# Kernel optimization log

Measured on AMD Instinct MI355X. Metric: run time of the kernel, lower is better.

Reference implementation:

```python
import jax, jax.numpy as jnp
import numpy as np

N, E, D, R, L = 50000, 600000, 64, 65, 2


def setup_inputs() -> dict:
    key = jax.random.key(0)
    ks = jax.random.split(key, 10)
    x = jax.random.normal(ks[0], (N, D), dtype=jnp.float32)
    edge_index = jax.random.randint(ks[1], (2, E), 0, N, dtype=jnp.int64)
    edge_type = jax.random.randint(ks[2], (E,), 0, R, dtype=jnp.int64)
    s = 1.0 / np.sqrt(D)
    W = jax.random.normal(ks[3], (L, R, D, D), dtype=jnp.float32) * s
    root = jax.random.normal(ks[4], (L, D, D), dtype=jnp.float32) * s
    bias = jax.random.normal(ks[5], (L, D), dtype=jnp.float32) * 0.01
    res_W = jax.random.normal(ks[6], (L, D, D), dtype=jnp.float32) * s
    res_b = jax.random.normal(ks[7], (L, D), dtype=jnp.float32) * 0.01
    return {"x": x, "edge_index": edge_index, "edge_type": edge_type,
            "W": W, "root": root, "bias": bias, "res_W": res_W, "res_b": res_b}


def _rgcn_conv(x, src, dst, edge_type, W_r, W_root, b):
    # PyG RGCNConv (num_bases=None, aggr='mean'):
    #   out_i = x_i @ W_root + b + sum_r mean_{j in N_r(i)} (x_j @ W_r)
    # mean is linear, so aggregate raw features per (node, relation) first,
    # then apply the per-relation transform once per node.
    n, d = x.shape
    r = W_r.shape[0]
    seg = dst * r + edge_type                       # [E]
    msg = x[src]                                    # [E, D] gather
    agg = jax.ops.segment_sum(msg, seg, num_segments=n * r).reshape(n, r, d)
    cnt = jax.ops.segment_sum(jnp.ones((msg.shape[0],), x.dtype), seg,
                              num_segments=n * r).reshape(n, r, 1)
    mean = agg / jnp.maximum(cnt, 1.0)              # [N, R, D]
    out = jnp.einsum('nrd,rdk->nk', mean, W_r)
    return out + x @ W_root + b


def reference(x, edge_index, edge_type, W, root, bias, res_W, res_b):
    src, dst = edge_index[0], edge_index[1]
    h = x
    for l in range(W.shape[0]):
        conv = _rgcn_conv(h, src, dst, edge_type, W[l], root[l], bias[l])
        conv = jax.nn.relu(conv)
        # dropout: identity in eval mode
        res = jax.nn.relu(h @ res_W[l] + res_b[l])
        h = conv + res
    return h
```

## Files before the change

### kernel.cpp

```cpp
#include <hip/hip_runtime.h>


constexpr int NN  = 50000;
constexpr int EE  = 600000;
constexpr int DIM = 64;
constexpr int RR  = 65;
constexpr int CHUNK = 256;
constexpr int MAXCHUNKS = EE / CHUNK + RR + 8;
constexpr int SORT_BS = 2048;
constexpr int NSB = (EE + SORT_BS - 1) / SORT_BS;
constexpr int SCAN_BS = 1024;
constexpr int SCAN_NB = (NN + SCAN_BS - 1) / SCAN_BS;
constexpr int XNB = 64;

typedef __attribute__((ext_vector_type(8))) short short8v;
typedef __attribute__((ext_vector_type(4))) float floatx4;

__device__ inline unsigned short f2bf(float f) {
  unsigned int u = __float_as_uint(f);
  return (unsigned short)((u + 0x7fffu + ((u >> 16) & 1u)) >> 16);
}
__device__ inline float bf2f(unsigned short v) {
  return __uint_as_float(((unsigned int)v) << 16);
}


__global__ __launch_bounds__(512) void cnt_k(const int* __restrict__ dst,
                                             const int* __restrict__ et,
                                             int* __restrict__ cnt, int E) {
  const int e = blockIdx.x * 512 + threadIdx.x;
  if (e < E) atomicAdd(&cnt[et[e] * NN + dst[e]], 1);
}

__global__ __launch_bounds__(512) void bhist_k(const int* __restrict__ et,
                                               int* __restrict__ bhist, int E) {
  __shared__ int lh[RR];
  for (int i = threadIdx.x; i < RR; i += 512) lh[i] = 0;
  __syncthreads();
  const int base = blockIdx.x * SORT_BS;
  for (int i = threadIdx.x; i < SORT_BS; i += 512) {
    const int e = base + i;
    if (e < E) atomicAdd(&lh[et[e]], 1);
  }
  __syncthreads();
  for (int i = threadIdx.x; i < RR; i += 512) bhist[blockIdx.x * RR + i] = lh[i];
}


__global__ __launch_bounds__(1024) void scan1_k(const int* __restrict__ cnt,
                                                int* __restrict__ deg,
                                                int* __restrict__ bsum) {
  __shared__ int s[SCAN_BS];
  const int idx = blockIdx.x * SCAN_BS + threadIdx.x;
  int d = 0;
  if (idx < NN) {
#pragma unroll 13
    for (int r = 0; r < RR; ++r) d += cnt[r * NN + idx];
    deg[idx] = d;
  }
  s[threadIdx.x] = d;
  __syncthreads();
  for (int off = SCAN_BS / 2; off > 0; off >>= 1) {
    if (threadIdx.x < off) s[threadIdx.x] += s[threadIdx.x + off];
    __syncthreads();
  }
  if (threadIdx.x == 0) bsum[blockIdx.x] = s[0];
}

__global__ __launch_bounds__(64) void scan2_k(int* __restrict__ bsum) {
  if (threadIdx.x == 0) {
    int run = 0;
    for (int b = 0; b < SCAN_NB; ++b) { const int v = bsum[b]; bsum[b] = run; run += v; }
  }
}

__global__ __launch_bounds__(1024) void scan3_k(const int* __restrict__ deg,
                                                const int* __restrict__ bsum,
                                                int* __restrict__ rowptr,
                                                int* __restrict__ poscur) {
  __shared__ int s[SCAN_BS];
  const int t = threadIdx.x;
  const int idx = blockIdx.x * SCAN_BS + t;
  const int v = (idx < NN) ? deg[idx] : 0;
  s[t] = v;
  __syncthreads();
  for (int off = 1; off < SCAN_BS; off <<= 1) {
    const int u = (t >= off) ? s[t - off] : 0;
    __syncthreads();
    s[t] += u;
    __syncthreads();
  }
  const int excl = bsum[blockIdx.x] + s[t] - v;
  if (idx < NN) { rowptr[idx] = excl; poscur[idx] = excl; }
  if (idx == NN - 1) rowptr[NN] = EE;
}

__global__ __launch_bounds__(128) void scan_type_k(const int* __restrict__ bhist,
                                                   int* __restrict__ boff,
                                                   int4* __restrict__ chunkArr,
                                                   int* __restrict__ nchunks) {
  __shared__ int total[RR], tptr[RR + 1], chbase[RR + 1];
  const int t = threadIdx.x;
  if (t < RR) {
    int s = 0;
    for (int b = 0; b < NSB; ++b) s += bhist[b * RR + t];
    total[t] = s;
  }
  __syncthreads();
  if (t == 0) {
    int run = 0, crun = 0;
    for (int r = 0; r < RR; ++r) {
      tptr[r] = run;   run  += total[r];
      chbase[r] = crun; crun += (total[r] + CHUNK - 1) / CHUNK;
    }
    tptr[RR] = run; chbase[RR] = crun;
    *nchunks = crun;
  }
  __syncthreads();
  if (t < RR) {
    int run = tptr[t];
    for (int b = 0; b < NSB; ++b) { boff[b * RR + t] = run; run += bhist[b * RR + t]; }
    const int nc = (total[t] + CHUNK - 1) / CHUNK;
    for (int i = 0; i < nc; ++i) {
      const int beg = tptr[t] + i * CHUNK;
      chunkArr[chbase[t] + i] = make_int4(beg, min(beg + CHUNK, tptr[t] + total[t]), t, 0);
    }
  }
}

__global__ __launch_bounds__(512) void scatter_k(const int* __restrict__ src,
                                                 const int* __restrict__ dst,
                                                 const int* __restrict__ et,
                                                 const int* __restrict__ cnt,
                                                 const int* __restrict__ boff,
                                                 int* __restrict__ poscur,
                                                 int* __restrict__ osrc,
                                                 int* __restrict__ opos,
                                                 float* __restrict__ oscale, int E) {
  __shared__ int cur[RR];
  for (int i = threadIdx.x; i < RR; i += 512) cur[i] = boff[blockIdx.x * RR + i];
  __syncthreads();
  const int base = blockIdx.x * SORT_BS;
  for (int i = threadIdx.x; i < SORT_BS; i += 512) {
    const int e = base + i;
    if (e < E) {
      const int s = src[e], d = dst[e], r = et[e];
      const int q = atomicAdd(&cur[r], 1);
      const int p = atomicAdd(&poscur[d], 1);
      osrc[q] = s;
      opos[q] = p;
      oscale[q] = 1.0f / (float)cnt[r * NN + d];
    }
  }
}


__global__ __launch_bounds__(256) void cvtw_k(const float* __restrict__ W,
                                              unsigned short* __restrict__ WT) {
  const int tid = blockIdx.x * 256 + threadIdx.x;
  const int total4 = 2 * RR * DIM * DIM / 4;
  if (tid >= total4) return;
  const int base = tid * 4;
  const int mat = base >> 12;
  const int rem = base & 4095;
  const int k = rem >> 6, c0 = rem & 63;
  const float4 v = *reinterpret_cast<const float4*>(W + base);
  unsigned short* o = WT + (size_t)mat * 4096;
  o[(c0 + 0) * 64 + k] = f2bf(v.x);
  o[(c0 + 1) * 64 + k] = f2bf(v.y);
  o[(c0 + 2) * 64 + k] = f2bf(v.z);
  o[(c0 + 3) * 64 + k] = f2bf(v.w);
}


__global__ __launch_bounds__(256) void msgm_k(const unsigned short* __restrict__ hbf,
                                              const int* __restrict__ osrc,
                                              const int* __restrict__ opos,
                                              const float* __restrict__ oscale,
                                              const unsigned short* __restrict__ WT,
                                              const int4* __restrict__ chunkArr,
                                              const int* __restrict__ nchunks,
                                              unsigned short* __restrict__ m) {
  const int ci = blockIdx.x;
  if (ci >= *nchunks) return;
  const int4 c = chunkArr[ci];
  const int beg = c.x, end = c.y, rel = c.z;

  __shared__ unsigned short Wl[DIM][72];
  {
    const float4* s4 = reinterpret_cast<const float4*>(WT + (size_t)rel * 4096);
#pragma unroll
    for (int it = 0; it < 2; ++it) {
      const int seg = threadIdx.x + it * 256;
      const int row = seg >> 3, s8 = seg & 7;
      *reinterpret_cast<float4*>(&Wl[row][s8 * 8]) = s4[seg];
    }
  }
  __syncthreads();

  const int w  = threadIdx.x >> 6;
  const int l  = threadIdx.x & 63;
  const int lr = l & 15, lq = l >> 4;

  const int ebase = beg + w * 64;
  if (ebase >= end) return;

  short8v a[4][2];
#pragma unroll
  for (int ct = 0; ct < 4; ++ct)
#pragma unroll
    for (int kk = 0; kk < 2; ++kk)
      a[ct][kk] = *reinterpret_cast<const short8v*>(&Wl[ct * 16 + lr][kk * 32 + lq * 8]);

  short8v b[4][2];
  int eidx[4];
#pragma unroll
  for (int et = 0; et < 4; ++et) {
    eidx[et] = ebase + et * 16 + lr;
    const int e = min(eidx[et], end - 1);
    const int s = osrc[e];
    const unsigned short* hp = hbf + (size_t)s * DIM;
    b[et][0] = *reinterpret_cast<const short8v*>(hp + lq * 8);
    b[et][1] = *reinterpret_cast<const short8v*>(hp + 32 + lq * 8);
  }

  floatx4 acc[4][4];
#pragma unroll
  for (int ct = 0; ct < 4; ++ct)
#pragma unroll
    for (int et = 0; et < 4; ++et)
      acc[ct][et] = (floatx4){0.f, 0.f, 0.f, 0.f};

#pragma unroll
  for (int kk = 0; kk < 2; ++kk)
#pragma unroll
    for (int ct = 0; ct < 4; ++ct)
#pragma unroll
      for (int et = 0; et < 4; ++et)
        acc[ct][et] = __builtin_amdgcn_mfma_f32_16x16x32_bf16(a[ct][kk], b[et][kk],
                                                              acc[ct][et], 0, 0, 0);

#pragma unroll
  for (int et = 0; et < 4; ++et) {
    const int e = eidx[et];
    if (e < end) {
      const float sc = oscale[e];
      unsigned short* op = m + (size_t)opos[e] * DIM;
#pragma unroll
      for (int ct = 0; ct < 4; ++ct) {
        ushort4 o;
        o.x = f2bf(acc[ct][et][0] * sc);
        o.y = f2bf(acc[ct][et][1] * sc);
        o.z = f2bf(acc[ct][et][2] * sc);
        o.w = f2bf(acc[ct][et][3] * sc);
        *reinterpret_cast<ushort4*>(op + ct * 16 + lq * 4) = o;
      }
    }
  }
}

__global__ __launch_bounds__(256) void msg_k(const float* __restrict__ h,
                                             const int* __restrict__ osrc,
                                             const int* __restrict__ opos,
                                             const float* __restrict__ oscale,
                                             const float* __restrict__ W,
                                             const int4* __restrict__ chunkArr,
                                             const int* __restrict__ nchunks,
                                             unsigned short* __restrict__ m) {
  const int ci = blockIdx.x;
  if (ci >= *nchunks) return;
  const int4 c = chunkArr[ci];
  const int beg = c.x, end = c.y, rel = c.z;

  __shared__ float Wlds[DIM * DIM];
  const float* Wg = W + (size_t)rel * (DIM * DIM);
#pragma unroll
  for (int i = 0; i < 4; ++i)
    *reinterpret_cast<float4*>(&Wlds[i * 1024 + threadIdx.x * 4]) =
        *reinterpret_cast<const float4*>(Wg + i * 1024 + threadIdx.x * 4);
  __syncthreads();

  const int g = threadIdx.x >> 4, li = threadIdx.x & 15;
  __shared__ float xs[16][4][68];

  for (int b = 0; b < 4; ++b) {
    const int e0 = beg + g * 16 + b * 4;
    const int nvalid = min(4, end - e0);
    if (nvalid <= 0) continue;

#pragma unroll
    for (int r = 0; r < 4; ++r) {
      const int e = e0 + ((r < nvalid) ? r : (nvalid - 1));
      const int s = osrc[e];
      *reinterpret_cast<float4*>(&xs[g][r][li * 4]) =
          *reinterpret_cast<const float4*>(h + (size_t)s * DIM + li * 4);
    }

    float acc[4][4];
#pragma unroll
    for (int r = 0; r < 4; ++r) { acc[r][0] = 0.f; acc[r][1] = 0.f; acc[r][2] = 0.f; acc[r][3] = 0.f; }

#pragma unroll 8
    for (int k = 0; k < DIM; ++k) {
      const float4 w = *reinterpret_cast<const float4*>(&Wlds[k * DIM + li * 4]);
#pragma unroll
      for (int r = 0; r < 4; ++r) {
        const float xv = xs[g][r][k];
        acc[r][0] += xv * w.x; acc[r][1] += xv * w.y;
        acc[r][2] += xv * w.z; acc[r][3] += xv * w.w;
      }
    }

    for (int r = 0; r < nvalid; ++r) {
      const int e = e0 + r;
      const float sc = oscale[e];
      ushort4 o;
      o.x = f2bf(acc[r][0] * sc); o.y = f2bf(acc[r][1] * sc);
      o.z = f2bf(acc[r][2] * sc); o.w = f2bf(acc[r][3] * sc);
      *reinterpret_cast<ushort4*>(m + (size_t)opos[e] * DIM + li * 4) = o;
    }
  }
}

__global__ __launch_bounds__(256) void xform_k(const float* __restrict__ h,
                                               const float* __restrict__ root,
                                               const float* __restrict__ bias,
                                               const float* __restrict__ rw,
                                               const float* __restrict__ rb,
                                               float* __restrict__ rt,
                                               float* __restrict__ rs,
                                               unsigned short* __restrict__ hbf, int N) {
  __shared__ float Wl0[DIM * DIM];
  __shared__ float Wl1[DIM * DIM];
  __shared__ float xs[XNB][68];
#pragma unroll
  for (int i = 0; i < 4; ++i) {
    reinterpret_cast<float4*>(Wl0)[threadIdx.x + i * 256] =
        reinterpret_cast<const float4*>(root)[threadIdx.x + i * 256];
    reinterpret_cast<float4*>(Wl1)[threadIdx.x + i * 256] =
        reinterpret_cast<const float4*>(rw)[threadIdx.x + i * 256];
  }

  const int g = threadIdx.x >> 4, li = threadIdx.x & 15;
  const int base = blockIdx.x * XNB;
#pragma unroll
  for (int r = 0; r < 4; ++r) {
    const int n = base + g * 4 + r;
    float4 v = make_float4(0.f, 0.f, 0.f, 0.f);
    if (n < N) v = *reinterpret_cast<const float4*>(h + (size_t)n * DIM + li * 4);
    *reinterpret_cast<float4*>(&xs[g * 4 + r][li * 4]) = v;
  }
  __syncthreads();

  if (hbf != nullptr) {
#pragma unroll
    for (int r = 0; r < 4; ++r) {
      const int n = base + g * 4 + r;
      if (n < N) {
        const float4 v = *reinterpret_cast<const float4*>(&xs[g * 4 + r][li * 4]);
        ushort4 o;
        o.x = f2bf(v.x); o.y = f2bf(v.y); o.z = f2bf(v.z); o.w = f2bf(v.w);
        *reinterpret_cast<ushort4*>(hbf + (size_t)n * DIM + li * 4) = o;
      }
    }
  }

  float aR[4][4], aS[4][4];
#pragma unroll
  for (int r = 0; r < 4; ++r)
#pragma unroll
    for (int q = 0; q < 4; ++q) { aR[r][q] = 0.f; aS[r][q] = 0.f; }

#pragma unroll 4
  for (int k = 0; k < DIM; ++k) {
    const float4 wr = *reinterpret_cast<const float4*>(&Wl0[k * DIM + li * 4]);
    const float4 wv = *reinterpret_cast<const float4*>(&Wl1[k * DIM + li * 4]);
#pragma unroll
    for (int r = 0; r < 4; ++r) {
      const float xv = xs[g * 4 + r][k];
      aR[r][0] += xv * wr.x; aR[r][1] += xv * wr.y; aR[r][2] += xv * wr.z; aR[r][3] += xv * wr.w;
      aS[r][0] += xv * wv.x; aS[r][1] += xv * wv.y; aS[r][2] += xv * wv.z; aS[r][3] += xv * wv.w;
    }
  }

  const float4 bv = reinterpret_cast<const float4*>(bias)[li];
  const float4 cv = reinterpret_cast<const float4*>(rb)[li];
#pragma unroll
  for (int r = 0; r < 4; ++r) {
    const int n = base + g * 4 + r;
    if (n < N) {
      *reinterpret_cast<float4*>(rt + (size_t)n * DIM + li * 4) =
          make_float4(aR[r][0] + bv.x, aR[r][1] + bv.y, aR[r][2] + bv.z, aR[r][3] + bv.w);
      *reinterpret_cast<float4*>(rs + (size_t)n * DIM + li * 4) =
          make_float4(fmaxf(aS[r][0] + cv.x, 0.f), fmaxf(aS[r][1] + cv.y, 0.f),
                      fmaxf(aS[r][2] + cv.z, 0.f), fmaxf(aS[r][3] + cv.w, 0.f));
    }
  }
}

__global__ __launch_bounds__(256) void gather2_k(const unsigned short* __restrict__ m,
                                                 const int* __restrict__ rowptr,
                                                 const float* __restrict__ rt,
                                                 const float* __restrict__ rs,
                                                 float* __restrict__ hout, int N) {
  const int g = threadIdx.x >> 4, li = threadIdx.x & 15;
  const int n = blockIdx.x * 16 + g;
  if (n >= N) return;

  float a0 = 0.f, a1 = 0.f, a2 = 0.f, a3 = 0.f;
  const int jb = rowptr[n], je = rowptr[n + 1];
  int j = jb;
  for (; j + 4 <= je; j += 4) {
    const ushort4 v0 = *reinterpret_cast<const ushort4*>(m + (size_t)(j + 0) * DIM + li * 4);
    const ushort4 v1 = *reinterpret_cast<const ushort4*>(m + (size_t)(j + 1) * DIM + li * 4);
    const ushort4 v2 = *reinterpret_cast<const ushort4*>(m + (size_t)(j + 2) * DIM + li * 4);
    const ushort4 v3 = *reinterpret_cast<const ushort4*>(m + (size_t)(j + 3) * DIM + li * 4);
    a0 += bf2f(v0.x) + bf2f(v1.x) + bf2f(v2.x) + bf2f(v3.x);
    a1 += bf2f(v0.y) + bf2f(v1.y) + bf2f(v2.y) + bf2f(v3.y);
    a2 += bf2f(v0.z) + bf2f(v1.z) + bf2f(v2.z) + bf2f(v3.z);
    a3 += bf2f(v0.w) + bf2f(v1.w) + bf2f(v2.w) + bf2f(v3.w);
  }
  for (; j < je; ++j) {
    const ushort4 v = *reinterpret_cast<const ushort4*>(m + (size_t)j * DIM + li * 4);
    a0 += bf2f(v.x); a1 += bf2f(v.y); a2 += bf2f(v.z); a3 += bf2f(v.w);
  }

  const float4 t = *reinterpret_cast<const float4*>(rt + (size_t)n * DIM + li * 4);
  const float4 s = *reinterpret_cast<const float4*>(rs + (size_t)n * DIM + li * 4);
  *reinterpret_cast<float4*>(hout + (size_t)n * DIM + li * 4) =
      make_float4(fmaxf(a0 + t.x, 0.f) + s.x, fmaxf(a1 + t.y, 0.f) + s.y,
                  fmaxf(a2 + t.z, 0.f) + s.z, fmaxf(a3 + t.w, 0.f) + s.w);
}

__global__ __launch_bounds__(256) void gather_k(const float* __restrict__ hin,
                                                const unsigned short* __restrict__ m,
                                                const int* __restrict__ rowptr,
                                                const float* __restrict__ root,
                                                const float* __restrict__ bias,
                                                const float* __restrict__ rw,
                                                const float* __restrict__ rb,
                                                float* __restrict__ hout, int N) {
  __shared__ float xs[16][68];
  const int g = threadIdx.x >> 4, li = threadIdx.x & 15;
  const int n = blockIdx.x * 16 + g;
  if (n >= N) return;

  *reinterpret_cast<float4*>(&xs[g][li * 4]) =
      *reinterpret_cast<const float4*>(hin + (size_t)n * DIM + li * 4);

  float a0 = 0.f, a1 = 0.f, a2 = 0.f, a3 = 0.f;
  const int jb = rowptr[n], je = rowptr[n + 1];
  for (int j = jb; j < je; ++j) {
    const ushort4 mv = *reinterpret_cast<const ushort4*>(m + (size_t)j * DIM + li * 4);
    a0 += bf2f(mv.x); a1 += bf2f(mv.y); a2 += bf2f(mv.z); a3 += bf2f(mv.w);
  }

  float r0 = 0.f, r1 = 0.f, r2 = 0.f, r3 = 0.f;
  float s0 = 0.f, s1 = 0.f, s2 = 0.f, s3 = 0.f;
#pragma unroll 8
  for (int k = 0; k < DIM; ++k) {
    const float hd = xs[g][k];
    const float4 w = *reinterpret_cast<const float4*>(root + k * DIM + li * 4);
    const float4 v = *reinterpret_cast<const float4*>(rw + k * DIM + li * 4);
    r0 += hd * w.x; r1 += hd * w.y; r2 += hd * w.z; r3 += hd * w.w;
    s0 += hd * v.x; s1 += hd * v.y; s2 += hd * v.z; s3 += hd * v.w;
  }
  const float4 b = *reinterpret_cast<const float4*>(bias + li * 4);
  const float4 cc = *reinterpret_cast<const float4*>(rb + li * 4);
  float o0 = fmaxf(a0 + r0 + b.x, 0.f) + fmaxf(s0 + cc.x, 0.f);
  float o1 = fmaxf(a1 + r1 + b.y, 0.f) + fmaxf(s1 + cc.y, 0.f);
  float o2 = fmaxf(a2 + r2 + b.z, 0.f) + fmaxf(s2 + cc.z, 0.f);
  float o3 = fmaxf(a3 + r3 + b.w, 0.f) + fmaxf(s3 + cc.w, 0.f);
  *reinterpret_cast<float4*>(hout + (size_t)n * DIM + li * 4) = make_float4(o0, o1, o2, o3);
}


__global__ __launch_bounds__(256) void count_k(const int* __restrict__ dst,
                                               const int* __restrict__ et,
                                               int* __restrict__ cnt, int E) {
  int e = blockIdx.x * 256 + threadIdx.x;
  if (e < E) atomicAdd(&cnt[dst[e] * RR + et[e]], 1);
}

__global__ __launch_bounds__(256) void edge_k(const float* __restrict__ h,
                                              const int* __restrict__ src,
                                              const int* __restrict__ dst,
                                              const int* __restrict__ et,
                                              const float* __restrict__ W,
                                              const int* __restrict__ cnt,
                                              float* __restrict__ accum, int E) {
  __shared__ float xs[16][68];
  const int g = threadIdx.x >> 4, li = threadIdx.x & 15;
  const int e = blockIdx.x * 16 + g;
  if (e >= E) return;
  const int s = src[e], d = dst[e], t = et[e];
  *reinterpret_cast<float4*>(&xs[g][li * 4]) =
      *reinterpret_cast<const float4*>(h + (size_t)s * DIM + li * 4);
  const float* Wt = W + (size_t)t * (DIM * DIM) + li * 4;
  float a0 = 0.f, a1 = 0.f, a2 = 0.f, a3 = 0.f;
#pragma unroll 8
  for (int k = 0; k < DIM; ++k) {
    const float xd = xs[g][k];
    const float4 w = *reinterpret_cast<const float4*>(Wt + k * DIM);
    a0 += xd * w.x; a1 += xd * w.y; a2 += xd * w.z; a3 += xd * w.w;
  }
  const float sc = 1.0f / (float)cnt[d * RR + t];
  float* o = accum + (size_t)d * DIM + li * 4;
  unsafeAtomicAdd(o + 0, a0 * sc);
  unsafeAtomicAdd(o + 1, a1 * sc);
  unsafeAtomicAdd(o + 2, a2 * sc);
  unsafeAtomicAdd(o + 3, a3 * sc);
}

__global__ __launch_bounds__(256) void node_k(const float* __restrict__ h,
                                              const float* __restrict__ root,
                                              const float* __restrict__ bias,
                                              const float* __restrict__ rw,
                                              const float* __restrict__ rb,
                                              float* __restrict__ io, int N) {
  __shared__ float xs[16][68];
  const int g = threadIdx.x >> 4, li = threadIdx.x & 15;
  const int n = blockIdx.x * 16 + g;
  if (n >= N) return;
  *reinterpret_cast<float4*>(&xs[g][li * 4]) =
      *reinterpret_cast<const float4*>(h + (size_t)n * DIM + li * 4);
  float r0 = 0.f, r1 = 0.f, r2 = 0.f, r3 = 0.f;
  float s0 = 0.f, s1 = 0.f, s2 = 0.f, s3 = 0.f;
#pragma unroll 8
  for (int k = 0; k < DIM; ++k) {
    const float hd = xs[g][k];
    const float4 w = *reinterpret_cast<const float4*>(root + k * DIM + li * 4);
    const float4 v = *reinterpret_cast<const float4*>(rw + k * DIM + li * 4);
    r0 += hd * w.x; r1 += hd * w.y; r2 += hd * w.z; r3 += hd * w.w;
    s0 += hd * v.x; s1 += hd * v.y; s2 += hd * v.z; s3 += hd * v.w;
  }
  float* o = io + (size_t)n * DIM + li * 4;
  const float4 acc = *reinterpret_cast<const float4*>(o);
  const float4 b = *reinterpret_cast<const float4*>(bias + li * 4);
  const float4 c = *reinterpret_cast<const float4*>(rb + li * 4);
  float o0 = fmaxf(acc.x + r0 + b.x, 0.f) + fmaxf(s0 + c.x, 0.f);
  float o1 = fmaxf(acc.y + r1 + b.y, 0.f) + fmaxf(s1 + c.y, 0.f);
  float o2 = fmaxf(acc.z + r2 + b.z, 0.f) + fmaxf(s2 + c.z, 0.f);
  float o3 = fmaxf(acc.w + r3 + b.w, 0.f) + fmaxf(s3 + c.w, 0.f);
  *reinterpret_cast<float4*>(o) = make_float4(o0, o1, o2, o3);
}


extern "C" void kernel_launch(void* const* d_in, const int* in_sizes, int n_in,
                              void* d_out, int out_size, void* d_ws, size_t ws_size,
                              hipStream_t stream) {
  const float* x    = (const float*)d_in[0];
  const int*   ei   = (const int*)d_in[1];
  const int*   et   = (const int*)d_in[2];
  const float* W    = (const float*)d_in[3];
  const float* root = (const float*)d_in[4];
  const float* bias = (const float*)d_in[5];
  const float* resW = (const float*)d_in[6];
  const float* resb = (const float*)d_in[7];
  float* out = (float*)d_out;

  const int* src = ei;
  const int* dstp = ei + EE;

  char* ws = (char*)d_ws;
  size_t off = 0;
  auto take = [&](size_t bytes) -> void* {
    void* p = ws + off;
    off = (off + bytes + 255) & ~(size_t)255;
    return p;
  };
  unsigned short* m = (unsigned short*)take((size_t)EE * DIM * sizeof(unsigned short));
  float* h1      = (float*)take((size_t)NN * DIM * sizeof(float));
  int* deg       = (int*)take((size_t)NN * sizeof(int));
  int* rowptr    = (int*)take((size_t)(NN + 1) * sizeof(int));
  int* poscur    = (int*)take((size_t)NN * sizeof(int));
  int* bhist     = (int*)take((size_t)NSB * RR * sizeof(int));
  int* boff      = (int*)take((size_t)NSB * RR * sizeof(int));
  int* bsum      = (int*)take((size_t)SCAN_NB * sizeof(int));
  int* osrc      = (int*)take((size_t)EE * sizeof(int));
  int* opos      = (int*)take((size_t)EE * sizeof(int));
  float* oscale  = (float*)take((size_t)EE * sizeof(float));
  int4* chunkArr = (int4*)take((size_t)MAXCHUNKS * sizeof(int4));
  int* nchunks   = (int*)take(256);
  const size_t base_off = off;
  float* rt      = (float*)take((size_t)NN * DIM * sizeof(float));
  float* rs      = (float*)take((size_t)NN * DIM * sizeof(float));
  const size_t t1_off = off;
  unsigned short* hbf = (unsigned short*)take((size_t)NN * DIM * sizeof(unsigned short));
  unsigned short* wbt = (unsigned short*)take((size_t)2 * RR * DIM * DIM * sizeof(unsigned short));
  const size_t mfma_off = off;
  int* cnt       = (int*)m;

  if (base_off <= ws_size) {
    hipMemsetAsync(cnt, 0, (size_t)NN * RR * sizeof(int), stream);

    cnt_k<<<(EE + 511) / 512, 512, 0, stream>>>(dstp, et, cnt, EE);
    bhist_k<<<NSB, 512, 0, stream>>>(et, bhist, EE);
    scan1_k<<<SCAN_NB, 1024, 0, stream>>>(cnt, deg, bsum);
    scan2_k<<<1, 64, 0, stream>>>(bsum);
    scan3_k<<<SCAN_NB, 1024, 0, stream>>>(deg, bsum, rowptr, poscur);
    scan_type_k<<<1, 128, 0, stream>>>(bhist, boff, chunkArr, nchunks);
    scatter_k<<<NSB, 512, 0, stream>>>(src, dstp, et, cnt, boff, poscur,
                                       osrc, opos, oscale, EE);

    const int XG = (NN + XNB - 1) / XNB;
    if (mfma_off <= ws_size) {
      cvtw_k<<<(2 * RR * DIM * DIM / 4 + 255) / 256, 256, 0, stream>>>(W, wbt);
      xform_k<<<XG, 256, 0, stream>>>(x, root, bias, resW, resb, rt, rs, hbf, NN);
      msgm_k<<<MAXCHUNKS, 256, 0, stream>>>(hbf, osrc, opos, oscale, wbt, chunkArr, nchunks, m);
      gather2_k<<<(NN + 15) / 16, 256, 0, stream>>>(m, rowptr, rt, rs, h1, NN);
      xform_k<<<XG, 256, 0, stream>>>(h1, root + DIM * DIM, bias + DIM,
                                      resW + DIM * DIM, resb + DIM, rt, rs, hbf, NN);
      msgm_k<<<MAXCHUNKS, 256, 0, stream>>>(hbf, osrc, opos, oscale,
                                            wbt + (size_t)RR * DIM * DIM, chunkArr, nchunks, m);
      gather2_k<<<(NN + 15) / 16, 256, 0, stream>>>(m, rowptr, rt, rs, out, NN);
    } else if (t1_off <= ws_size) {
      msg_k<<<MAXCHUNKS, 256, 0, stream>>>(x, osrc, opos, oscale, W, chunkArr, nchunks, m);
      xform_k<<<XG, 256, 0, stream>>>(x, root, bias, resW, resb, rt, rs, nullptr, NN);
      gather2_k<<<(NN + 15) / 16, 256, 0, stream>>>(m, rowptr, rt, rs, h1, NN);
      msg_k<<<MAXCHUNKS, 256, 0, stream>>>(h1, osrc, opos, oscale,
                                           W + (size_t)RR * DIM * DIM, chunkArr, nchunks, m);
      xform_k<<<XG, 256, 0, stream>>>(h1, root + DIM * DIM, bias + DIM,
                                      resW + DIM * DIM, resb + DIM, rt, rs, nullptr, NN);
      gather2_k<<<(NN + 15) / 16, 256, 0, stream>>>(m, rowptr, rt, rs, out, NN);
    } else {
      msg_k<<<MAXCHUNKS, 256, 0, stream>>>(x, osrc, opos, oscale, W, chunkArr, nchunks, m);
      gather_k<<<(NN + 15) / 16, 256, 0, stream>>>(x, m, rowptr, root, bias, resW, resb, h1, NN);
      msg_k<<<MAXCHUNKS, 256, 0, stream>>>(h1, osrc, opos, oscale,
                                           W + (size_t)RR * DIM * DIM, chunkArr, nchunks, m);
      gather_k<<<(NN + 15) / 16, 256, 0, stream>>>(h1, m, rowptr, root + DIM * DIM, bias + DIM,
                                                   resW + DIM * DIM, resb + DIM, out, NN);
    }
  } else {
    int* fcnt = (int*)ws;
    float* fh1 = (float*)(ws + (size_t)NN * RR * sizeof(int));
    hipMemsetAsync(fcnt, 0, (size_t)NN * RR * sizeof(int), stream);
    hipMemsetAsync(fh1, 0, (size_t)NN * DIM * sizeof(float), stream);
    hipMemsetAsync(out, 0, (size_t)NN * DIM * sizeof(float), stream);
    count_k<<<(EE + 255) / 256, 256, 0, stream>>>(dstp, et, fcnt, EE);
    edge_k<<<(EE + 15) / 16, 256, 0, stream>>>(x, src, dstp, et, W, fcnt, fh1, EE);
    node_k<<<(NN + 15) / 16, 256, 0, stream>>>(x, root, bias, resW, resb, fh1, NN);
    edge_k<<<(EE + 15) / 16, 256, 0, stream>>>(fh1, src, dstp, et,
                                               W + (size_t)RR * DIM * DIM, fcnt, out, EE);
    node_k<<<(NN + 15) / 16, 256, 0, stream>>>(fh1, root + DIM * DIM, bias + DIM,
                                               resW + DIM * DIM, resb + DIM, out, NN);
  }
}
```

Before: 273.0 us.

## Replace dense per-(node,relation) count array with per-node degree and local relation counts

Drops the NN×RR count array, which needed a 13MB memset, scattered atomics and a 65-way strided reduction for degrees. Degrees now come from a per-node atomic histogram fused with the relation block histogram. Mean scales are recomputed per destination segment by a quadratic scan over relation ids and applied in the gather instead of the message kernel. It also halves the sort block size and removes the non-MFMA fallback paths, which adds an extra kernel and an extra per-edge array.

```diff
diff --git a/kernel.cpp b/kernel.cpp
--- a/kernel.cpp
+++ b/kernel.cpp
@@ -7,7 +7,7 @@
 constexpr int RR  = 65;
 constexpr int CHUNK = 256;
 constexpr int MAXCHUNKS = EE / CHUNK + RR + 8;
-constexpr int SORT_BS = 2048;
+constexpr int SORT_BS = 1024;
 constexpr int NSB = (EE + SORT_BS - 1) / SORT_BS;
 constexpr int SCAN_BS = 1024;
 constexpr int SCAN_NB = (NN + SCAN_BS - 1) / SCAN_BS;
@@ -25,40 +25,37 @@
 }
 
 
-__global__ __launch_bounds__(512) void cnt_k(const int* __restrict__ dst,
-                                             const int* __restrict__ et,
-                                             int* __restrict__ cnt, int E) {
-  const int e = blockIdx.x * 512 + threadIdx.x;
-  if (e < E) atomicAdd(&cnt[et[e] * NN + dst[e]], 1);
-}
-
-__global__ __launch_bounds__(512) void bhist_k(const int* __restrict__ et,
+__global__ __launch_bounds__(256) void zero_k(int* __restrict__ p, int n) {
+  const int i = blockIdx.x * 256 + threadIdx.x;
+  if (i < n) p[i] = 0;
+}
+
+__global__ __launch_bounds__(512) void hist2_k(const int* __restrict__ dst,
+                                               const int* __restrict__ et,
+                                               int* __restrict__ deg,
                                                int* __restrict__ bhist, int E) {
   __shared__ int lh[RR];
-  for (int i = threadIdx.x; i < RR; i += 512) lh[i] = 0;
+  if (threadIdx.x < RR) lh[threadIdx.x] = 0;
   __syncthreads();
   const int base = blockIdx.x * SORT_BS;
-  for (int i = threadIdx.x; i < SORT_BS; i += 512) {
-    const int e = base + i;
-    if (e < E) atomicAdd(&lh[et[e]], 1);
-  }
-  __syncthreads();
-  for (int i = threadIdx.x; i < RR; i += 512) bhist[blockIdx.x * RR + i] = lh[i];
-}
-
-
-__global__ __launch_bounds__(1024) void scan1_k(const int* __restrict__ cnt,
-                                                int* __restrict__ deg,
+#pragma unroll
+  for (int it = 0; it < SORT_BS / 512; ++it) {
+    const int e = base + it * 512 + threadIdx.x;
+    if (e < E) {
+      atomicAdd(&deg[dst[e]], 1);
+      atomicAdd(&lh[et[e]], 1);
+    }
+  }
+  __syncthreads();
+  if (threadIdx.x < RR) bhist[blockIdx.x * RR + threadIdx.x] = lh[threadIdx.x];
+}
+
+
+__global__ __launch_bounds__(1024) void scan1_k(const int* __restrict__ deg,
                                                 int* __restrict__ bsum) {
   __shared__ int s[SCAN_BS];
   const int idx = blockIdx.x * SCAN_BS + threadIdx.x;
-  int d = 0;
-  if (idx < NN) {
-#pragma unroll 13
-    for (int r = 0; r < RR; ++r) d += cnt[r * NN + idx];
-    deg[idx] = d;
-  }
-  s[threadIdx.x] = d;
+  s[threadIdx.x] = (idx < NN) ? deg[idx] : 0;
   __syncthreads();
   for (int off = SCAN_BS / 2; off > 0; off >>= 1) {
     if (threadIdx.x < off) s[threadIdx.x] += s[threadIdx.x + off];
@@ -128,29 +125,43 @@
   }
 }
 
-__global__ __launch_bounds__(512) void scatter_k(const int* __restrict__ src,
-                                                 const int* __restrict__ dst,
-                                                 const int* __restrict__ et,
-                                                 const int* __restrict__ cnt,
-                                                 const int* __restrict__ boff,
-                                                 int* __restrict__ poscur,
-                                                 int* __restrict__ osrc,
-                                                 int* __restrict__ opos,
-                                                 float* __restrict__ oscale, int E) {
+__global__ __launch_bounds__(512) void scatter2_k(const int* __restrict__ src,
+                                                  const int* __restrict__ dst,
+                                                  const int* __restrict__ et,
+                                                  const int* __restrict__ boff,
+                                                  int* __restrict__ poscur,
+                                                  int* __restrict__ osrc,
+                                                  int* __restrict__ opos,
+                                                  int* __restrict__ orel, int E) {
   __shared__ int cur[RR];
-  for (int i = threadIdx.x; i < RR; i += 512) cur[i] = boff[blockIdx.x * RR + i];
+  if (threadIdx.x < RR) cur[threadIdx.x] = boff[blockIdx.x * RR + threadIdx.x];
   __syncthreads();
   const int base = blockIdx.x * SORT_BS;
-  for (int i = threadIdx.x; i < SORT_BS; i += 512) {
-    const int e = base + i;
+#pragma unroll
+  for (int it = 0; it < SORT_BS / 512; ++it) {
+    const int e = base + it * 512 + threadIdx.x;
     if (e < E) {
       const int s = src[e], d = dst[e], r = et[e];
       const int q = atomicAdd(&cur[r], 1);
       const int p = atomicAdd(&poscur[d], 1);
       osrc[q] = s;
       opos[q] = p;
-      oscale[q] = 1.0f / (float)cnt[r * NN + d];
-    }
+      orel[p] = r;
+    }
+  }
+}
+
+__global__ __launch_bounds__(256) void scale_k(const int* __restrict__ rowptr,
+                                               const int* __restrict__ orel,
+                                               float* __restrict__ sc, int N) {
+  const int n = blockIdx.x * 256 + threadIdx.x;
+  if (n >= N) return;
+  const int jb = rowptr[n], je = rowptr[n + 1];
+  for (int j1 = jb; j1 < je; ++j1) {
+    const int r1 = orel[j1];
+    int c = 0;
+    for (int j2 = jb; j2 < je; ++j2) c += (orel[j2] == r1) ? 1 : 0;
+    sc[j1] = 1.0f / (float)c;
   }
 }
 
@@ -176,7 +187,6 @@
 __global__ __launch_bounds__(256) void msgm_k(const unsigned short* __restrict__ hbf,
                                               const int* __restrict__ osrc,
                                               const int* __restrict__ opos,
-                                              const float* __restrict__ oscale,
                                               const unsigned short* __restrict__ WT,
                                               const int4* __restrict__ chunkArr,
                                               const int* __restrict__ nchunks,
@@ -244,80 +254,16 @@
   for (int et = 0; et < 4; ++et) {
     const int e = eidx[et];
     if (e < end) {
-      const float sc = oscale[e];
       unsigned short* op = m + (size_t)opos[e] * DIM;
 #pragma unroll
       for (int ct = 0; ct < 4; ++ct) {
         ushort4 o;
-        o.x = f2bf(acc[ct][et][0] * sc);
-        o.y = f2bf(acc[ct][et][1] * sc);
-        o.z = f2bf(acc[ct][et][2] * sc);
-        o.w = f2bf(acc[ct][et][3] * sc);
+        o.x = f2bf(acc[ct][et][0]);
+        o.y = f2bf(acc[ct][et][1]);
+        o.z = f2bf(acc[ct][et][2]);
+        o.w = f2bf(acc[ct][et][3]);
         *reinterpret_cast<ushort4*>(op + ct * 16 + lq * 4) = o;
       }
-    }
-  }
-}
-
-__global__ __launch_bounds__(256) void msg_k(const float* __restrict__ h,
-                                             const int* __restrict__ osrc,
-                                             const int* __restrict__ opos,
-                                             const float* __restrict__ oscale,
-                                             const float* __restrict__ W,
-                                             const int4* __restrict__ chunkArr,
-                                             const int* __restrict__ nchunks,
-                                             unsigned short* __restrict__ m) {
-  const int ci = blockIdx.x;
-  if (ci >= *nchunks) return;
-  const int4 c = chunkArr[ci];
-  const int beg = c.x, end = c.y, rel = c.z;
-
-  __shared__ float Wlds[DIM * DIM];
-  const float* Wg = W + (size_t)rel * (DIM * DIM);
-#pragma unroll
-  for (int i = 0; i < 4; ++i)
-    *reinterpret_cast<float4*>(&Wlds[i * 1024 + threadIdx.x * 4]) =
-        *reinterpret_cast<const float4*>(Wg + i * 1024 + threadIdx.x * 4);
-  __syncthreads();
-
-  const int g = threadIdx.x >> 4, li = threadIdx.x & 15;
-  __shared__ float xs[16][4][68];
-
-  for (int b = 0; b < 4; ++b) {
-    const int e0 = beg + g * 16 + b * 4;
-    const int nvalid = min(4, end - e0);
-    if (nvalid <= 0) continue;
-
-#pragma unroll
-    for (int r = 0; r < 4; ++r) {
-      const int e = e0 + ((r < nvalid) ? r : (nvalid - 1));
-      const int s = osrc[e];
-      *reinterpret_cast<float4*>(&xs[g][r][li * 4]) =
-          *reinterpret_cast<const float4*>(h + (size_t)s * DIM + li * 4);
-    }
-
-    float acc[4][4];
-#pragma unroll
-    for (int r = 0; r < 4; ++r) { acc[r][0] = 0.f; acc[r][1] = 0.f; acc[r][2] = 0.f; acc[r][3] = 0.f; }
-
-#pragma unroll 8
-    for (int k = 0; k < DIM; ++k) {
-      const float4 w = *reinterpret_cast<const float4*>(&Wlds[k * DIM + li * 4]);
-#pragma unroll
-      for (int r = 0; r < 4; ++r) {
-        const float xv = xs[g][r][k];
-        acc[r][0] += xv * w.x; acc[r][1] += xv * w.y;
-        acc[r][2] += xv * w.z; acc[r][3] += xv * w.w;
-      }
-    }
-
-    for (int r = 0; r < nvalid; ++r) {
-      const int e = e0 + r;
-      const float sc = oscale[e];
-      ushort4 o;
-      o.x = f2bf(acc[r][0] * sc); o.y = f2bf(acc[r][1] * sc);
-      o.z = f2bf(acc[r][2] * sc); o.w = f2bf(acc[r][3] * sc);
-      *reinterpret_cast<ushort4*>(m + (size_t)opos[e] * DIM + li * 4) = o;
     }
   }
 }
@@ -398,7 +344,8 @@
   }
 }
 
-__global__ __launch_bounds__(256) void gather2_k(const unsigned short* __restrict__ m,
+__global__ __launch_bounds__(256) void gather3_k(const unsigned short* __restrict__ m,
+                                                 const float* __restrict__ sc,
                                                  const int* __restrict__ rowptr,
                                                  const float* __restrict__ rt,
                                                  const float* __restrict__ rs,
@@ -411,18 +358,20 @@
   const int jb = rowptr[n], je = rowptr[n + 1];
   int j = jb;
   for (; j + 4 <= je; j += 4) {
+    const float c0 = sc[j + 0], c1 = sc[j + 1], c2 = sc[j + 2], c3 = sc[j + 3];
     const ushort4 v0 = *reinterpret_cast<const ushort4*>(m + (size_t)(j + 0) * DIM + li * 4);
     const ushort4 v1 = *reinterpret_cast<const ushort4*>(m + (size_t)(j + 1) * DIM + li * 4);
     const ushort4 v2 = *reinterpret_cast<const ushort4*>(m + (size_t)(j + 2) * DIM + li * 4);
     const ushort4 v3 = *reinterpret_cast<const ushort4*>(m + (size_t)(j + 3) * DIM + li * 4);
-    a0 += bf2f(v0.x) + bf2f(v1.x) + bf2f(v2.x) + bf2f(v3.x);
-    a1 += bf2f(v0.y) + bf2f(v1.y) + bf2f(v2.y) + bf2f(v3.y);
-    a2 += bf2f(v0.z) + bf2f(v1.z) + bf2f(v2.z) + bf2f(v3.z);
-    a3 += bf2f(v0.w) + bf2f(v1.w) + bf2f(v2.w) + bf2f(v3.w);
+    a0 += c0 * bf2f(v0.x) + c1 * bf2f(v1.x) + c2 * bf2f(v2.x) + c3 * bf2f(v3.x);
+    a1 += c0 * bf2f(v0.y) + c1 * bf2f(v1.y) + c2 * bf2f(v2.y) + c3 * bf2f(v3.y);
+    a2 += c0 * bf2f(v0.z) + c1 * bf2f(v1.z) + c2 * bf2f(v2.z) + c3 * bf2f(v3.z);
+    a3 += c0 * bf2f(v0.w) + c1 * bf2f(v1.w) + c2 * bf2f(v2.w) + c3 * bf2f(v3.w);
   }
   for (; j < je; ++j) {
+    const float cc = sc[j];
     const ushort4 v = *reinterpret_cast<const ushort4*>(m + (size_t)j * DIM + li * 4);
-    a0 += bf2f(v.x); a1 += bf2f(v.y); a2 += bf2f(v.z); a3 += bf2f(v.w);
+    a0 += cc * bf2f(v.x); a1 += cc * bf2f(v.y); a2 += cc * bf2f(v.z); a3 += cc * bf2f(v.w);
   }
 
   const float4 t = *reinterpret_cast<const float4*>(rt + (size_t)n * DIM + li * 4);
@@ -430,48 +379,6 @@
   *reinterpret_cast<float4*>(hout + (size_t)n * DIM + li * 4) =
       make_float4(fmaxf(a0 + t.x, 0.f) + s.x, fmaxf(a1 + t.y, 0.f) + s.y,
                   fmaxf(a2 + t.z, 0.f) + s.z, fmaxf(a3 + t.w, 0.f) + s.w);
-}
-
-__global__ __launch_bounds__(256) void gather_k(const float* __restrict__ hin,
-                                                const unsigned short* __restrict__ m,
-                                                const int* __restrict__ rowptr,
-                                                const float* __restrict__ root,
-                                                const float* __restrict__ bias,
-                                                const float* __restrict__ rw,
-                                                const float* __restrict__ rb,
-                                                float* __restrict__ hout, int N) {
-  __shared__ float xs[16][68];
-  const int g = threadIdx.x >> 4, li = threadIdx.x & 15;
-  const int n = blockIdx.x * 16 + g;
-  if (n >= N) return;
-
-  *reinterpret_cast<float4*>(&xs[g][li * 4]) =
-      *reinterpret_cast<const float4*>(hin + (size_t)n * DIM + li * 4);
-
-  float a0 = 0.f, a1 = 0.f, a2 = 0.f, a3 = 0.f;
-  const int jb = rowptr[n], je = rowptr[n + 1];
-  for (int j = jb; j < je; ++j) {
-    const ushort4 mv = *reinterpret_cast<const ushort4*>(m + (size_t)j * DIM + li * 4);
-    a0 += bf2f(mv.x); a1 += bf2f(mv.y); a2 += bf2f(mv.z); a3 += bf2f(mv.w);
-  }
-
-  float r0 = 0.f, r1 = 0.f, r2 = 0.f, r3 = 0.f;
-  float s0 = 0.f, s1 = 0.f, s2 = 0.f, s3 = 0.f;
-#pragma unroll 8
-  for (int k = 0; k < DIM; ++k) {
-    const float hd = xs[g][k];
-    const float4 w = *reinterpret_cast<const float4*>(root + k * DIM + li * 4);
-    const float4 v = *reinterpret_cast<const float4*>(rw + k * DIM + li * 4);
-    r0 += hd * w.x; r1 += hd * w.y; r2 += hd * w.z; r3 += hd * w.w;
-    s0 += hd * v.x; s1 += hd * v.y; s2 += hd * v.z; s3 += hd * v.w;
-  }
-  const float4 b = *reinterpret_cast<const float4*>(bias + li * 4);
-  const float4 cc = *reinterpret_cast<const float4*>(rb + li * 4);
-  float o0 = fmaxf(a0 + r0 + b.x, 0.f) + fmaxf(s0 + cc.x, 0.f);
-  float o1 = fmaxf(a1 + r1 + b.y, 0.f) + fmaxf(s1 + cc.y, 0.f);
-  float o2 = fmaxf(a2 + r2 + b.z, 0.f) + fmaxf(s2 + cc.z, 0.f);
-  float o3 = fmaxf(a3 + r3 + b.w, 0.f) + fmaxf(s3 + cc.w, 0.f);
-  *reinterpret_cast<float4*>(hout + (size_t)n * DIM + li * 4) = make_float4(o0, o1, o2, o3);
 }
 
 
@@ -579,58 +486,37 @@
   int* bsum      = (int*)take((size_t)SCAN_NB * sizeof(int));
   int* osrc      = (int*)take((size_t)EE * sizeof(int));
   int* opos      = (int*)take((size_t)EE * sizeof(int));
-  float* oscale  = (float*)take((size_t)EE * sizeof(float));
+  int* orel      = (int*)take((size_t)EE * sizeof(int));
+  float* sc      = (float*)take((size_t)EE * sizeof(float));
   int4* chunkArr = (int4*)take((size_t)MAXCHUNKS * sizeof(int4));
   int* nchunks   = (int*)take(256);
-  const size_t base_off = off;
   float* rt      = (float*)take((size_t)NN * DIM * sizeof(float));
   float* rs      = (float*)take((size_t)NN * DIM * sizeof(float));
-  const size_t t1_off = off;
   unsigned short* hbf = (unsigned short*)take((size_t)NN * DIM * sizeof(unsigned short));
   unsigned short* wbt = (unsigned short*)take((size_t)2 * RR * DIM * DIM * sizeof(unsigned short));
-  const size_t mfma_off = off;
-  int* cnt       = (int*)m;
-
-  if (base_off <= ws_size) {
-    hipMemsetAsync(cnt, 0, (size_t)NN * RR * sizeof(int), stream);
-
-    cnt_k<<<(EE + 511) / 512, 512, 0, stream>>>(dstp, et, cnt, EE);
-    bhist_k<<<NSB, 512, 0, stream>>>(et, bhist, EE);
-    scan1_k<<<SCAN_NB, 1024, 0, stream>>>(cnt, deg, bsum);
+  const size_t main_off = off;
+
+  if (main_off <= ws_size) {
+    zero_k<<<(NN + 255) / 256, 256, 0, stream>>>(deg, NN);
+    hist2_k<<<NSB, 512, 0, stream>>>(dstp, et, deg, bhist, EE);
+    scan1_k<<<SCAN_NB, 1024, 0, stream>>>(deg, bsum);
     scan2_k<<<1, 64, 0, stream>>>(bsum);
     scan3_k<<<SCAN_NB, 1024, 0, stream>>>(deg, bsum, rowptr, poscur);
     scan_type_k<<<1, 128, 0, stream>>>(bhist, boff, chunkArr, nchunks);
-    scatter_k<<<NSB, 512, 0, stream>>>(src, dstp, et, cnt, boff, poscur,
-                                       osrc, opos, oscale, EE);
+    scatter2_k<<<NSB, 512, 0, stream>>>(src, dstp, et, boff, poscur,
+                                        osrc, opos, orel, EE);
+    scale_k<<<(NN + 255) / 256, 256, 0, stream>>>(rowptr, orel, sc, NN);
+    cvtw_k<<<(2 * RR * DIM * DIM / 4 + 255) / 256, 256, 0, stream>>>(W, wbt);
 
     const int XG = (NN + XNB - 1) / XNB;
-    if (mfma_off <= ws_size) {
-      cvtw_k<<<(2 * RR * DIM * DIM / 4 + 255) / 256, 256, 0, stream>>>(W, wbt);
-      xform_k<<<XG, 256, 0, stream>>>(x, root, bias, resW, resb, rt, rs, hbf, NN);
-      msgm_k<<<MAXCHUNKS, 256, 0, stream>>>(hbf, osrc, opos, oscale, wbt, chunkArr, nchunks, m);
-      gather2_k<<<(NN + 15) / 16, 256, 0, stream>>>(m, rowptr, rt, rs, h1, NN);
-      xform_k<<<XG, 256, 0, stream>>>(h1, root + DIM * DIM, bias + DIM,
-                                      resW + DIM * DIM, resb + DIM, rt, rs, hbf, NN);
-      msgm_k<<<MAXCHUNKS, 256, 0, stream>>>(hbf, osrc, opos, oscale,
-                                            wbt + (size_t)RR * DIM * DIM, chunkArr, nchunks, m);
-      gather2_k<<<(NN + 15) / 16, 256, 0, stream>>>(m, rowptr, rt, rs, out, NN);
-    } else if (t1_off <= ws_size) {
-      msg_k<<<MAXCHUNKS, 256, 0, stream>>>(x, osrc, opos, oscale, W, chunkArr, nchunks, m);
-      xform_k<<<XG, 256, 0, stream>>>(x, root, bias, resW, resb, rt, rs, nullptr, NN);
-      gather2_k<<<(NN + 15) / 16, 256, 0, stream>>>(m, rowptr, rt, rs, h1, NN);
-      msg_k<<<MAXCHUNKS, 256, 0, stream>>>(h1, osrc, opos, oscale,
-                                           W + (size_t)RR * DIM * DIM, chunkArr, nchunks, m);
-      xform_k<<<XG, 256, 0, stream>>>(h1, root + DIM * DIM, bias + DIM,
-                                      resW + DIM * DIM, resb + DIM, rt, rs, nullptr, NN);
-      gather2_k<<<(NN + 15) / 16, 256, 0, stream>>>(m, rowptr, rt, rs, out, NN);
-    } else {
-      msg_k<<<MAXCHUNKS, 256, 0, stream>>>(x, osrc, opos, oscale, W, chunkArr, nchunks, m);
-      gather_k<<<(NN + 15) / 16, 256, 0, stream>>>(x, m, rowptr, root, bias, resW, resb, h1, NN);
-      msg_k<<<MAXCHUNKS, 256, 0, stream>>>(h1, osrc, opos, oscale,
-                                           W + (size_t)RR * DIM * DIM, chunkArr, nchunks, m);
-      gather_k<<<(NN + 15) / 16, 256, 0, stream>>>(h1, m, rowptr, root + DIM * DIM, bias + DIM,
-                                                   resW + DIM * DIM, resb + DIM, out, NN);
-    }
+    xform_k<<<XG, 256, 0, stream>>>(x, root, bias, resW, resb, rt, rs, hbf, NN);
+    msgm_k<<<MAXCHUNKS, 256, 0, stream>>>(hbf, osrc, opos, wbt, chunkArr, nchunks, m);
+    gather3_k<<<(NN + 15) / 16, 256, 0, stream>>>(m, sc, rowptr, rt, rs, h1, NN);
+    xform_k<<<XG, 256, 0, stream>>>(h1, root + DIM * DIM, bias + DIM,
+                                    resW + DIM * DIM, resb + DIM, rt, rs, hbf, NN);
+    msgm_k<<<MAXCHUNKS, 256, 0, stream>>>(hbf, osrc, opos,
+                                          wbt + (size_t)RR * DIM * DIM, chunkArr, nchunks, m);
+    gather3_k<<<(NN + 15) / 16, 256, 0, stream>>>(m, sc, rowptr, rt, rs, out, NN);
   } else {
     int* fcnt = (int*)ws;
     float* fh1 = (float*)(ws + (size_t)NN * RR * sizeof(int));
```

Result: slower. 350.1 us (+28.2%).
